# Kernel optimization log

Measured on AMD Instinct MI355X. Metric: run time of the kernel, lower is better.

The kernel has to match this reference:

```python
import jax, jax.numpy as jnp
import numpy as np

B, N, D = 16, 2048, 256  # batch (pairs*2), num_keypoints, descriptor_dim


def setup_inputs() -> dict:
    key = jax.random.key(0)
    k1, k2, k3, k4 = jax.random.split(key, 4)
    descriptors = jax.random.normal(k1, (B, N, D), dtype=jnp.float32)
    mask = jax.random.randint(k2, (B, N), 0, 2, dtype=jnp.int32)
    proj_w = jax.random.normal(k3, (D, D), dtype=jnp.float32) * 0.02
    proj_b = jnp.zeros((D,), dtype=jnp.float32)
    match_w = jax.random.normal(k4, (1, D), dtype=jnp.float32) * 0.02
    match_b = jnp.zeros((1,), dtype=jnp.float32)
    return {"descriptors": descriptors, "mask": mask, "proj_w": proj_w,
            "proj_b": proj_b, "match_w": match_w, "match_b": match_b}


def reference(descriptors, mask, proj_w, proj_b, match_w, match_b):
    batch, n, d = descriptors.shape
    pairs = batch // 2
    # final projection + temperature scaling
    m_desc = (descriptors @ proj_w.T + proj_b) / jnp.asarray(d, descriptors.dtype) ** 0.25
    m_desc = m_desc.reshape(pairs, 2, n, d)
    # similarity: [pairs, n0, n1]
    similarity = jnp.einsum('bnd,bmd->bnm', m_desc[:, 0], m_desc[:, 1])
    mask_p = mask.reshape(pairs, 2, n)
    pair_mask = mask_p[:, 0][:, :, None] * mask_p[:, 1][:, None, :]
    neg_min = jnp.finfo(similarity.dtype).min
    similarity = jnp.where(pair_mask == 0, neg_min, similarity)
    # matchability logits: [B, n, 1] -> split per pair
    matchability = (descriptors @ match_w.T + match_b).reshape(pairs, 2, n)
    m0 = matchability[:, 0]  # [pairs, n]
    m1 = matchability[:, 1]  # [pairs, n]
    certainties = jax.nn.log_sigmoid(m0)[:, :, None] + jax.nn.log_sigmoid(m1)[:, None, :]
    scores0 = jax.nn.log_softmax(similarity, axis=2)
    scores1 = jax.nn.log_softmax(similarity, axis=1)
    inner = scores0 + scores1 + certainties
    scores = jnp.zeros((pairs, n + 1, n + 1), dtype=similarity.dtype)
    scores = scores.at[:, :n, :n].set(inner)
    scores = scores.at[:, :-1, -1].set(jax.nn.log_sigmoid(-m0))
    scores = scores.at[:, -1, :-1].set(jax.nn.log_sigmoid(-m1))
    return scores
```

## Files before the change

kernel.cpp:

```cpp
#include <hip/hip_runtime.h>
#include <math.h>

typedef unsigned short u16;
typedef __attribute__((ext_vector_type(8))) short bf16x8;
typedef __attribute__((ext_vector_type(4))) float f32x4;

#define N 2048
#define D 256
#define PAIRS 8
#define NO 2049
#define NEGMIN  -3.40282347e38f
#define MASKVAL -3.0e38f
#define LDA 72
#define LDST 136

#define WS_LS0   0
#define WS_LS1   (1*PAIRS*N)
#define WS_LSN0  (2*PAIRS*N)
#define WS_LSN1  (3*PAIRS*N)
#define WS_RMAX  (4*PAIRS*N)
#define WS_RLSE  (5*PAIRS*N)
#define WS_CMAX  (6*PAIRS*N)
#define WS_CLSE  (7*PAIRS*N)
#define WS_RPM   (8*PAIRS*N)
#define WS_RPS   (WS_RPM + PAIRS*16*N)
#define WS_CPM   (WS_RPS + PAIRS*16*N)
#define WS_CPS   (WS_CPM + PAIRS*16*N)
#define WS_F_COUNT (WS_CPS + PAIRS*16*N)

__device__ __forceinline__ float b2f(u16 u) {
    return __uint_as_float(((unsigned)u) << 16);
}
__device__ __forceinline__ u16 f2b(float f) {
    unsigned x = __float_as_uint(f);
    x += 0x7FFFu + ((x >> 16) & 1u);
    return (u16)(x >> 16);
}
__device__ __forceinline__ unsigned pk2(float a, float b) {
    return (unsigned)f2b(a) | ((unsigned)f2b(b) << 16);
}
__device__ __forceinline__ float logsig(float x) {
    return fminf(x, 0.f) - log1pf(expf(-fabsf(x)));
}
__device__ __forceinline__ void online1(float& m, float& s, float x) {
    float nm = fmaxf(m, x);
    float e = __expf(fminf(m, x) - nm);
    s = (x > m) ? s * e + 1.f : s + e;
    m = nm;
}
__device__ __forceinline__ void onmerge(float& m, float& s, float om, float os) {
    float nm = fmaxf(m, om);
    s = s * __expf(m - nm) + os * __expf(om - nm);
    m = nm;
}
__device__ __forceinline__ void gl_lds16(const u16* g, u16* l) {
    __builtin_amdgcn_global_load_lds(
        (const __attribute__((address_space(1))) unsigned*)(const void*)g,
        (__attribute__((address_space(3))) unsigned*)(void*)l, 16, 0, 0);
}

__global__ __launch_bounds__(256) void k_proj_mfma(const float* __restrict__ A,
                                                   const float* __restrict__ W,
                                                   const float* __restrict__ bias,
                                                   const float* __restrict__ mw,
                                                   const float* __restrict__ mb,
                                                   u16* __restrict__ mdesc,
                                                   float* __restrict__ wsf) {
    __shared__ union {
        struct { u16 A[128 * LDA]; u16 B[128 * LDA]; } t;
        u16 stage[128][LDST];
    } sh;
    int r0 = blockIdx.x * 128, c0 = blockIdx.y * 128;
    int tid = threadIdx.x;
    int w = tid >> 6, lane = tid & 63;
    int ln = lane & 15, q = lane >> 4;
    int wr0 = (w >> 1) * 64, wc0 = (w & 1) * 64;
    f32x4 zero = {0.f, 0.f, 0.f, 0.f};
    f32x4 acc[4][4];
    #pragma unroll
    for (int a = 0; a < 4; ++a)
        #pragma unroll
        for (int b = 0; b < 4; ++b) acc[a][b] = zero;
    float mdot[4] = {0.f, 0.f, 0.f, 0.f};
    int domatch = (blockIdx.y == 0);

    for (int kb = 0; kb < D; kb += 64) {
        __syncthreads();
        #pragma unroll
        for (int t = 0; t < 4; ++t) {
            int c = t * 256 + tid;
            int row = c >> 3, part = c & 7;
            const float* ap = A + (size_t)(r0 + row) * D + kb + part * 8;
            float4 f0 = *(const float4*)ap;
            float4 f1 = *(const float4*)(ap + 4);
            uint4 va;
            va.x = pk2(f0.x, f0.y); va.y = pk2(f0.z, f0.w);
            va.z = pk2(f1.x, f1.y); va.w = pk2(f1.z, f1.w);
            *(uint4*)&sh.t.A[row * LDA + part * 8] = va;
            if (domatch) {
                float4 w0 = *(const float4*)(mw + kb + part * 8);
                float4 w1 = *(const float4*)(mw + kb + part * 8 + 4);
                mdot[t] += f0.x*w0.x + f0.y*w0.y + f0.z*w0.z + f0.w*w0.w
                         + f1.x*w1.x + f1.y*w1.y + f1.z*w1.z + f1.w*w1.w;
            }
            const float* bp = W + (size_t)(c0 + row) * D + kb + part * 8;
            float4 g0 = *(const float4*)bp;
            float4 g1 = *(const float4*)(bp + 4);
            uint4 vb;
            vb.x = pk2(g0.x, g0.y); vb.y = pk2(g0.z, g0.w);
            vb.z = pk2(g1.x, g1.y); vb.w = pk2(g1.z, g1.w);
            *(uint4*)&sh.t.B[row * LDA + part * 8] = vb;
        }
        __syncthreads();
        #pragma unroll
        for (int kk = 0; kk < 64; kk += 32) {
            bf16x8 af[4], bf[4];
            #pragma unroll
            for (int ri = 0; ri < 4; ++ri)
                af[ri] = *(const bf16x8*)&sh.t.A[(wr0 + ri*16 + ln) * LDA + kk + q*8];
            #pragma unroll
            for (int ci = 0; ci < 4; ++ci)
                bf[ci] = *(const bf16x8*)&sh.t.B[(wc0 + ci*16 + ln) * LDA + kk + q*8];
            #pragma unroll
            for (int ri = 0; ri < 4; ++ri)
                #pragma unroll
                for (int ci = 0; ci < 4; ++ci)
                    acc[ri][ci] = __builtin_amdgcn_mfma_f32_16x16x32_bf16(af[ri], bf[ci], acc[ri][ci], 0, 0, 0);
        }
    }
    if (domatch) {
        #pragma unroll
        for (int t = 0; t < 4; ++t) {
            float s = mdot[t];
            s += __shfl_xor(s, 1, 64);
            s += __shfl_xor(s, 2, 64);
            s += __shfl_xor(s, 4, 64);
            if ((tid & 7) == 0) {
                int row_g = r0 + t * 32 + (tid >> 3);
                float m = s + mb[0];
                int b = row_g >> 11;
                int i = row_g & (N - 1);
                int pp = b >> 1, sid = b & 1;
                float ls = logsig(m), lsn = logsig(-m);
                if (sid == 0) { wsf[WS_LS0 + pp*N + i] = ls; wsf[WS_LSN0 + pp*N + i] = lsn; }
                else          { wsf[WS_LS1 + pp*N + i] = ls; wsf[WS_LSN1 + pp*N + i] = lsn; }
            }
        }
    }
    __syncthreads();
    #pragma unroll
    for (int ri = 0; ri < 4; ++ri) {
        #pragma unroll
        for (int reg = 0; reg < 4; ++reg) {
            int row_l = wr0 + ri*16 + q*4 + reg;
            #pragma unroll
            for (int ci = 0; ci < 4; ++ci) {
                int col = c0 + wc0 + ci*16 + ln;
                float v = (acc[ri][ci][reg] + bias[col]) * 0.25f;
                sh.stage[row_l][wc0 + ci*16 + ln] = f2b(v);
            }
        }
    }
    __syncthreads();
    {
        int row_l = tid >> 1, half = tid & 1;
        u16* dp = mdesc + (size_t)(r0 + row_l) * D + c0 + half * 64;
        const u16* lp = &sh.stage[row_l][half * 64];
        #pragma unroll
        for (int i = 0; i < 8; ++i)
            *(uint4*)(dp + i * 8) = *(const uint4*)(lp + i * 8);
    }
}

__global__ __launch_bounds__(256) void k_sim_mfma(const u16* __restrict__ mdesc,
                                                  const int* __restrict__ mask,
                                                  u16* __restrict__ sim,
                                                  float* __restrict__ wsf) {
    __shared__ union {
        u16 lds[4][128 * 64];
        u16 stage[128][LDST];
    } sh;
    __shared__ float rpm[128][2], rps[128][2];
    __shared__ float cpm[128][2], cps[128][2];
    int p = blockIdx.z;
    const u16* Am = mdesc + (size_t)(2*p) * N * D;
    const u16* Bm = mdesc + (size_t)(2*p + 1) * N * D;
    int r0 = blockIdx.x * 128, c0 = blockIdx.y * 128;
    int tid = threadIdx.x;
    int w = tid >> 6, lane = tid & 63;
    int ln = lane & 15, q = lane >> 4;
    int wr0 = (w >> 1) * 64, wc0 = (w & 1) * 64;
    int rsub = lane >> 3;
    int scol = (((lane & 7) ^ rsub) << 3);
    f32x4 zero = {0.f, 0.f, 0.f, 0.f};
    f32x4 acc[4][4];
    #pragma unroll
    for (int a = 0; a < 4; ++a)
        #pragma unroll
        for (int b = 0; b < 4; ++b) acc[a][b] = zero;

    #define STAGE(t_, bufi_) do {                                               \
        int kb_ = (t_) * 64;                                                    \
        u16* Ad_ = &sh.lds[(bufi_)*2][0];                                       \
        u16* Bd_ = &sh.lds[(bufi_)*2+1][0];                                     \
        _Pragma("unroll")                                                       \
        for (int j_ = 0; j_ < 4; ++j_) {                                        \
            int row_ = w * 32 + j_ * 8 + rsub;                                  \
            gl_lds16(Am + (size_t)(r0 + row_) * D + kb_ + scol,                 \
                     Ad_ + (w * 32 + j_ * 8) * 64);                             \
            gl_lds16(Bm + (size_t)(c0 + row_) * D + kb_ + scol,                 \
                     Bd_ + (w * 32 + j_ * 8) * 64);                             \
        }                                                                       \
    } while (0)

    STAGE(0, 0);
    __syncthreads();
    #pragma unroll
    for (int t = 0; t < 4; ++t) {
        int cur = t & 1;
        if (t < 3) STAGE(t + 1, cur ^ 1);
        const char* Abase = (const char*)&sh.lds[cur*2][0];
        const char* Bbase = (const char*)&sh.lds[cur*2+1][0];
        #pragma unroll
        for (int kk = 0; kk < 64; kk += 32) {
            bf16x8 af[4], bf[4];
            int cbase = kk * 2 + q * 16;
            int cswz = cbase ^ ((ln & 7) << 4);
            #pragma unroll
            for (int ri = 0; ri < 4; ++ri) {
                int row = wr0 + ri*16 + ln;
                af[ri] = *(const bf16x8*)(Abase + row * 128 + cswz);
            }
            #pragma unroll
            for (int ci = 0; ci < 4; ++ci) {
                int row = wc0 + ci*16 + ln;
                bf[ci] = *(const bf16x8*)(Bbase + row * 128 + cswz);
            }
            #pragma unroll
            for (int ri = 0; ri < 4; ++ri)
                #pragma unroll
                for (int ci = 0; ci < 4; ++ci)
                    acc[ri][ci] = __builtin_amdgcn_mfma_f32_16x16x32_bf16(af[ri], bf[ci], acc[ri][ci], 0, 0, 0);
        }
        __syncthreads();
    }
    #undef STAGE

    const int* m0 = mask + (size_t)(2*p) * N;
    const int* m1 = mask + (size_t)(2*p + 1) * N;
    int mcol[4];
    #pragma unroll
    for (int ci = 0; ci < 4; ++ci) mcol[ci] = m1[c0 + wc0 + ci*16 + ln];
    #pragma unroll
    for (int ri = 0; ri < 4; ++ri) {
        #pragma unroll
        for (int reg = 0; reg < 4; ++reg) {
            int row_l = wr0 + ri*16 + q*4 + reg;
            int mr = m0[r0 + row_l];
            #pragma unroll
            for (int ci = 0; ci < 4; ++ci) {
                float v = (mr && mcol[ci]) ? acc[ri][ci][reg] : MASKVAL;
                acc[ri][ci][reg] = v;
                sh.stage[row_l][wc0 + ci*16 + ln] = f2b(v);
            }
        }
    }
    #pragma unroll
    for (int ri = 0; ri < 4; ++ri) {
        #pragma unroll
        for (int reg = 0; reg < 4; ++reg) {
            float x0 = acc[ri][0][reg], x1 = acc[ri][1][reg];
            float x2 = acc[ri][2][reg], x3 = acc[ri][3][reg];
            float m = fmaxf(fmaxf(x0, x1), fmaxf(x2, x3));
            #pragma unroll
            for (int off = 1; off <= 8; off <<= 1)
                m = fmaxf(m, __shfl_xor(m, off, 64));
            float s = __expf(x0 - m) + __expf(x1 - m) + __expf(x2 - m) + __expf(x3 - m);
            #pragma unroll
            for (int off = 1; off <= 8; off <<= 1)
                s += __shfl_xor(s, off, 64);
            if (ln == 0) {
                int rl = wr0 + ri*16 + q*4 + reg;
                rpm[rl][w & 1] = m; rps[rl][w & 1] = s;
            }
        }
    }
    #pragma unroll
    for (int ci = 0; ci < 4; ++ci) {
        float m = acc[0][ci][0];
        #pragma unroll
        for (int ri = 0; ri < 4; ++ri)
            #pragma unroll
            for (int reg = 0; reg < 4; ++reg)
                if (!(ri == 0 && reg == 0)) m = fmaxf(m, acc[ri][ci][reg]);
        #pragma unroll
        for (int off = 16; off <= 32; off <<= 1)
            m = fmaxf(m, __shfl_xor(m, off, 64));
        float s = 0.f;
        #pragma unroll
        for (int ri = 0; ri < 4; ++ri)
            #pragma unroll
            for (int reg = 0; reg < 4; ++reg)
                s += __expf(acc[ri][ci][reg] - m);
        #pragma unroll
        for (int off = 16; off <= 32; off <<= 1)
            s += __shfl_xor(s, off, 64);
        if (q == 0) {
            int cl = wc0 + ci*16 + ln;
            cpm[cl][w >> 1] = m; cps[cl][w >> 1] = s;
        }
    }
    __syncthreads();
    {
        int row_l = tid >> 1, half = tid & 1;
        u16* sp = sim + ((size_t)p * N + r0 + row_l) * N + c0 + half * 64;
        const u16* lp = &sh.stage[row_l][half * 64];
        #pragma unroll
        for (int i = 0; i < 8; ++i)
            *(uint4*)(sp + i * 8) = *(const uint4*)(lp + i * 8);
    }
    if (tid < 128) {
        float m = rpm[tid][0], s = rps[tid][0];
        onmerge(m, s, rpm[tid][1], rps[tid][1]);
        size_t o = (size_t)(p * 16 + blockIdx.y) * N + r0 + tid;
        wsf[WS_RPM + o] = m; wsf[WS_RPS + o] = s;
    } else {
        int c = tid - 128;
        float m = cpm[c][0], s = cps[c][0];
        onmerge(m, s, cpm[c][1], cps[c][1]);
        size_t o = (size_t)(p * 16 + blockIdx.x) * N + c0 + c;
        wsf[WS_CPM + o] = m;
        wsf[WS_CPS + o] = s;
    }
}

__global__ __launch_bounds__(256) void k_red(float* __restrict__ wsf) {
    int i = blockIdx.x * 256 + threadIdx.x;
    int p = blockIdx.y;
    float m = wsf[WS_CPM + (size_t)(p*16) * N + i];
    float s = wsf[WS_CPS + (size_t)(p*16) * N + i];
    #pragma unroll
    for (int rb = 1; rb < 16; ++rb)
        onmerge(m, s, wsf[WS_CPM + (size_t)(p*16 + rb) * N + i],
                      wsf[WS_CPS + (size_t)(p*16 + rb) * N + i]);
    wsf[WS_CMAX + p * N + i] = m;
    wsf[WS_CLSE + p * N + i] = logf(s);
}

__global__ __launch_bounds__(256) void k_final(u16* __restrict__ out,
                                               const u16* __restrict__ sim,
                                               const float* __restrict__ wsf) {
    int strip = blockIdx.x;
    int p = blockIdx.y;
    int tid = threadIdx.x;
    __shared__ float rm_l[8], rl_l[8], l0_l[8], ln0_l[8];
    if (tid < 128) {
        int r = tid >> 4, cb = tid & 15;
        int i = strip * 8 + r;
        if (i < N) {
            float m = wsf[WS_RPM + (size_t)(p*16 + cb) * N + i];
            float sv = wsf[WS_RPS + (size_t)(p*16 + cb) * N + i];
            #pragma unroll
            for (int off = 1; off <= 8; off <<= 1) {
                float om = __shfl_xor(m, off, 64);
                float os = __shfl_xor(sv, off, 64);
                onmerge(m, sv, om, os);
            }
            if (cb == 0) {
                rm_l[r]  = m;
                rl_l[r]  = logf(sv);
                l0_l[r]  = wsf[WS_LS0  + p*N + i];
                ln0_l[r] = wsf[WS_LSN0 + p*N + i];
            }
        }
    }
    __syncthreads();
    unsigned* up = (unsigned*)out;
    #pragma unroll
    for (int k = 0; k < 4; ++k) {
        int kk = k * 256 + tid;
        int jc = 2 * kk;
        float cm0 = wsf[WS_CMAX + p*N + jc];
        float cl0 = wsf[WS_CLSE + p*N + jc];
        float s10 = wsf[WS_LS1  + p*N + jc];
        float cm1 = wsf[WS_CMAX + p*N + jc + 1];
        float cl1 = wsf[WS_CLSE + p*N + jc + 1];
        float s11 = wsf[WS_LS1  + p*N + jc + 1];
        float cm2 = 0.f, cl2 = 0.f, s12 = 0.f;
        if (jc + 2 < N) {
            cm2 = wsf[WS_CMAX + p*N + jc + 2];
            cl2 = wsf[WS_CLSE + p*N + jc + 2];
            s12 = wsf[WS_LS1  + p*N + jc + 2];
        }
        for (int r = 0; r < 8; ++r) {
            int i = strip * 8 + r;
            if (i > N) break;
            size_t B0 = ((size_t)p * NO + i) * NO;
            int head = (p + i) & 1;
            size_t U0 = (B0 + head) >> 1;
            if (i == N) {
                int j0 = 2*kk + head;
                float o0 = (j0 < N) ? wsf[WS_LSN1 + p*N + j0] : 0.f;
                int j1 = j0 + 1;
                float o1 = (j1 < N) ? wsf[WS_LSN1 + p*N + j1] : 0.f;
                up[U0 + kk] = pk2(o0, o1);
                if (tid == 0 && k == 0) {
                    if (head) out[B0] = f2b(wsf[WS_LSN1 + p*N]);
                    else      out[B0 + N] = 0;
                }
                continue;
            }
            float rm = rm_l[r], rl = rl_l[r], l0 = l0_l[r], ln0 = ln0_l[r];
            const u16* srow = sim + ((size_t)p * N + i) * N;
            unsigned a = *(const unsigned*)(srow + jc);
            float o0, o1;
            if (head) {
                float x0 = b2f((u16)(a >> 16));
                float a0 = (x0 - rm) - rl;
                float b0 = (x0 - cm1) - cl1;
                o0 = fmaxf(fmaxf(a0 + b0, MASKVAL) + (l0 + s11), MASKVAL);
                if (jc + 2 < N) {
                    float x1 = b2f(srow[jc + 2]);
                    float a1 = (x1 - rm) - rl;
                    float b1 = (x1 - cm2) - cl2;
                    o1 = fmaxf(fmaxf(a1 + b1, MASKVAL) + (l0 + s12), MASKVAL);
                } else {
                    o1 = ln0;
                }
            } else {
                float x0 = b2f((u16)a);
                float a0 = (x0 - rm) - rl;
                float b0 = (x0 - cm0) - cl0;
                o0 = fmaxf(fmaxf(a0 + b0, MASKVAL) + (l0 + s10), MASKVAL);
                float x1 = b2f((u16)(a >> 16));
                float a1 = (x1 - rm) - rl;
                float b1 = (x1 - cm1) - cl1;
                o1 = fmaxf(fmaxf(a1 + b1, MASKVAL) + (l0 + s11), MASKVAL);
            }
            up[U0 + kk] = pk2(o0, o1);
            if (tid == 0 && k == 0) {
                if (head) {
                    float x = b2f(srow[0]);
                    float aa = (x - rm) - rl;
                    float bb = (x - wsf[WS_CMAX + p*N]) - wsf[WS_CLSE + p*N];
                    out[B0] = f2b(fmaxf(fmaxf(aa + bb, MASKVAL) + (l0 + wsf[WS_LS1 + p*N]), MASKVAL));
                } else {
                    out[B0 + N] = f2b(ln0);
                }
            }
        }
    }
}

extern "C" void kernel_launch(void* const* d_in, const int* in_sizes, int n_in,
                              void* d_out, int out_size, void* d_ws, size_t ws_size,
                              hipStream_t stream) {
    const float* desc    = (const float*)d_in[0];
    const int*   mask    = (const int*)d_in[1];
    const float* proj_w  = (const float*)d_in[2];
    const float* proj_b  = (const float*)d_in[3];
    const float* match_w = (const float*)d_in[4];
    const float* match_b = (const float*)d_in[5];
    u16*   out = (u16*)d_out;
    float* wsf = (float*)d_ws;
    u16*   mdesc = (u16*)((char*)d_ws + (size_t)WS_F_COUNT * sizeof(float));
    u16*   simw  = mdesc + (size_t)16 * N * D;

    k_proj_mfma<<<dim3(256, 2),    256, 0, stream>>>(desc, proj_w, proj_b, match_w, match_b, mdesc, wsf);
    k_sim_mfma <<<dim3(16, 16, 8), 256, 0, stream>>>(mdesc, mask, simw, wsf);
    k_red      <<<dim3(8, 8),      256, 0, stream>>>(wsf);
    k_final    <<<dim3(257, 8),    256, 0, stream>>>(out, simw, wsf);
}
```

Baseline: 275.9 us.

## Precompute packed row/column stats and stage final output through LDS

The row-partial merge moves from k_final into k_red, which now also writes packed per-row (neg max-lse, ls0, lsn0) and per-column (neg max-lse, ls1) records so k_final loads vectorised structs instead of many scattered scalars. k_final reads the bf16 similarity with 16-byte loads, computes 8 outputs per thread, stages them in LDS to handle the odd row alignment of the 2049-wide output, then writes aligned 32-bit stores. The last output row is handled by a dedicated strip branch. This adds LDS use and a barrier per block and makes k_red do more work.

```diff
diff --git a/kernel.cpp b/kernel.cpp
--- a/kernel.cpp
+++ b/kernel.cpp
@@ -18,15 +18,13 @@
 #define WS_LS1   (1*PAIRS*N)
 #define WS_LSN0  (2*PAIRS*N)
 #define WS_LSN1  (3*PAIRS*N)
-#define WS_RMAX  (4*PAIRS*N)
-#define WS_RLSE  (5*PAIRS*N)
-#define WS_CMAX  (6*PAIRS*N)
-#define WS_CLSE  (7*PAIRS*N)
+#define WS_CST   (6*PAIRS*N)
 #define WS_RPM   (8*PAIRS*N)
 #define WS_RPS   (WS_RPM + PAIRS*16*N)
 #define WS_CPM   (WS_RPS + PAIRS*16*N)
 #define WS_CPS   (WS_CPM + PAIRS*16*N)
-#define WS_F_COUNT (WS_CPS + PAIRS*16*N)
+#define WS_ROW   (WS_CPS + PAIRS*16*N)
+#define WS_F_COUNT (WS_ROW + 4*PAIRS*N)
 
 __device__ __forceinline__ float b2f(u16 u) {
     return __uint_as_float(((unsigned)u) << 16);
@@ -41,12 +39,6 @@
 }
 __device__ __forceinline__ float logsig(float x) {
     return fminf(x, 0.f) - log1pf(expf(-fabsf(x)));
-}
-__device__ __forceinline__ void online1(float& m, float& s, float x) {
-    float nm = fmaxf(m, x);
-    float e = __expf(fminf(m, x) - nm);
-    s = (x > m) ? s * e + 1.f : s + e;
-    m = nm;
 }
 __device__ __forceinline__ void onmerge(float& m, float& s, float om, float os) {
     float nm = fmaxf(m, om);
@@ -343,8 +335,22 @@
     for (int rb = 1; rb < 16; ++rb)
         onmerge(m, s, wsf[WS_CPM + (size_t)(p*16 + rb) * N + i],
                       wsf[WS_CPS + (size_t)(p*16 + rb) * N + i]);
-    wsf[WS_CMAX + p * N + i] = m;
-    wsf[WS_CLSE + p * N + i] = logf(s);
+    float2 cpack;
+    cpack.x = -m - logf(s);
+    cpack.y = wsf[WS_LS1 + p*N + i];
+    *(float2*)&wsf[WS_CST + ((size_t)p * N + i) * 2] = cpack;
+    float rm = wsf[WS_RPM + (size_t)(p*16) * N + i];
+    float rs = wsf[WS_RPS + (size_t)(p*16) * N + i];
+    #pragma unroll
+    for (int rb = 1; rb < 16; ++rb)
+        onmerge(rm, rs, wsf[WS_RPM + (size_t)(p*16 + rb) * N + i],
+                        wsf[WS_RPS + (size_t)(p*16 + rb) * N + i]);
+    float4 rpack;
+    rpack.x = -rm - logf(rs);
+    rpack.y = wsf[WS_LS0  + p*N + i];
+    rpack.z = wsf[WS_LSN0 + p*N + i];
+    rpack.w = 0.f;
+    *(float4*)&wsf[WS_ROW + ((size_t)p * N + i) * 4] = rpack;
 }
 
 __global__ __launch_bounds__(256) void k_final(u16* __restrict__ out,
@@ -353,101 +359,79 @@
     int strip = blockIdx.x;
     int p = blockIdx.y;
     int tid = threadIdx.x;
-    __shared__ float rm_l[8], rl_l[8], l0_l[8], ln0_l[8];
-    if (tid < 128) {
-        int r = tid >> 4, cb = tid & 15;
+    unsigned* up = (unsigned*)out;
+    if (strip == 256) {
+        int head = p & 1;
+        size_t B0 = ((size_t)p * NO + N) * NO;
+        size_t U0 = (B0 + head) >> 1;
+        const float* lsn1 = wsf + WS_LSN1 + p * N;
+        #pragma unroll
+        for (int k = 0; k < 4; ++k) {
+            int kk = k * 256 + tid;
+            int j0 = head + 2 * kk;
+            float o0 = (j0 < N) ? lsn1[j0] : 0.f;
+            float o1 = (j0 + 1 < N) ? lsn1[j0 + 1] : 0.f;
+            up[U0 + kk] = pk2(o0, o1);
+        }
+        if (tid == 0) {
+            if (head) out[B0] = f2b(lsn1[0]);
+            else      out[B0 + N] = 0;
+        }
+        return;
+    }
+    __shared__ u16 stg[8][2052];
+    int c8 = tid * 8;
+    const float* cst = wsf + WS_CST + ((size_t)p * N + c8) * 2;
+    float4 cs[4];
+    #pragma unroll
+    for (int k = 0; k < 4; ++k) cs[k] = *(const float4*)(cst + 4 * k);
+    #pragma unroll
+    for (int r = 0; r < 8; ++r) {
         int i = strip * 8 + r;
-        if (i < N) {
-            float m = wsf[WS_RPM + (size_t)(p*16 + cb) * N + i];
-            float sv = wsf[WS_RPS + (size_t)(p*16 + cb) * N + i];
-            #pragma unroll
-            for (int off = 1; off <= 8; off <<= 1) {
-                float om = __shfl_xor(m, off, 64);
-                float os = __shfl_xor(sv, off, 64);
-                onmerge(m, sv, om, os);
-            }
-            if (cb == 0) {
-                rm_l[r]  = m;
-                rl_l[r]  = logf(sv);
-                l0_l[r]  = wsf[WS_LS0  + p*N + i];
-                ln0_l[r] = wsf[WS_LSN0 + p*N + i];
-            }
-        }
+        int head = (p + i) & 1;
+        float4 rsv = *(const float4*)&wsf[WS_ROW + ((size_t)p * N + i) * 4];
+        float rc = rsv.x, l0 = rsv.y, ln0 = rsv.z;
+        uint4 v = *(const uint4*)(sim + ((size_t)p * N + i) * N + c8);
+        unsigned vv[4] = {v.x, v.y, v.z, v.w};
+        float o[8];
+        #pragma unroll
+        for (int k = 0; k < 8; ++k) {
+            float x = b2f((u16)(vv[k >> 1] >> ((k & 1) * 16)));
+            float cA = ((const float*)&cs[0])[2 * k];
+            float s1 = ((const float*)&cs[0])[2 * k + 1];
+            float t = (x + rc) + (x + cA);
+            o[k] = fmaxf(fmaxf(t, MASKVAL) + (l0 + s1), MASKVAL);
+        }
+        if (!head) {
+            uint4 wv;
+            wv.x = pk2(o[0], o[1]); wv.y = pk2(o[2], o[3]);
+            wv.z = pk2(o[4], o[5]); wv.w = pk2(o[6], o[7]);
+            *(uint4*)&stg[r][c8] = wv;
+        } else {
+            stg[r][c8 + 1] = f2b(o[0]);
+            *(unsigned*)&stg[r][c8 + 2] = pk2(o[1], o[2]);
+            *(unsigned*)&stg[r][c8 + 4] = pk2(o[3], o[4]);
+            *(unsigned*)&stg[r][c8 + 6] = pk2(o[5], o[6]);
+            stg[r][c8 + 8] = f2b(o[7]);
+        }
+        if (tid == 255) stg[r][2048 + head] = f2b(ln0);
     }
     __syncthreads();
-    unsigned* up = (unsigned*)out;
-    #pragma unroll
-    for (int k = 0; k < 4; ++k) {
-        int kk = k * 256 + tid;
-        int jc = 2 * kk;
-        float cm0 = wsf[WS_CMAX + p*N + jc];
-        float cl0 = wsf[WS_CLSE + p*N + jc];
-        float s10 = wsf[WS_LS1  + p*N + jc];
-        float cm1 = wsf[WS_CMAX + p*N + jc + 1];
-        float cl1 = wsf[WS_CLSE + p*N + jc + 1];
-        float s11 = wsf[WS_LS1  + p*N + jc + 1];
-        float cm2 = 0.f, cl2 = 0.f, s12 = 0.f;
-        if (jc + 2 < N) {
-            cm2 = wsf[WS_CMAX + p*N + jc + 2];
-            cl2 = wsf[WS_CLSE + p*N + jc + 2];
-            s12 = wsf[WS_LS1  + p*N + jc + 2];
-        }
-        for (int r = 0; r < 8; ++r) {
-            int i = strip * 8 + r;
-            if (i > N) break;
-            size_t B0 = ((size_t)p * NO + i) * NO;
-            int head = (p + i) & 1;
-            size_t U0 = (B0 + head) >> 1;
-            if (i == N) {
-                int j0 = 2*kk + head;
-                float o0 = (j0 < N) ? wsf[WS_LSN1 + p*N + j0] : 0.f;
-                int j1 = j0 + 1;
-                float o1 = (j1 < N) ? wsf[WS_LSN1 + p*N + j1] : 0.f;
-                up[U0 + kk] = pk2(o0, o1);
-                if (tid == 0 && k == 0) {
-                    if (head) out[B0] = f2b(wsf[WS_LSN1 + p*N]);
-                    else      out[B0 + N] = 0;
-                }
-                continue;
-            }
-            float rm = rm_l[r], rl = rl_l[r], l0 = l0_l[r], ln0 = ln0_l[r];
-            const u16* srow = sim + ((size_t)p * N + i) * N;
-            unsigned a = *(const unsigned*)(srow + jc);
-            float o0, o1;
-            if (head) {
-                float x0 = b2f((u16)(a >> 16));
-                float a0 = (x0 - rm) - rl;
-                float b0 = (x0 - cm1) - cl1;
-                o0 = fmaxf(fmaxf(a0 + b0, MASKVAL) + (l0 + s11), MASKVAL);
-                if (jc + 2 < N) {
-                    float x1 = b2f(srow[jc + 2]);
-                    float a1 = (x1 - rm) - rl;
-                    float b1 = (x1 - cm2) - cl2;
-                    o1 = fmaxf(fmaxf(a1 + b1, MASKVAL) + (l0 + s12), MASKVAL);
-                } else {
-                    o1 = ln0;
-                }
-            } else {
-                float x0 = b2f((u16)a);
-                float a0 = (x0 - rm) - rl;
-                float b0 = (x0 - cm0) - cl0;
-                o0 = fmaxf(fmaxf(a0 + b0, MASKVAL) + (l0 + s10), MASKVAL);
-                float x1 = b2f((u16)(a >> 16));
-                float a1 = (x1 - rm) - rl;
-                float b1 = (x1 - cm1) - cl1;
-                o1 = fmaxf(fmaxf(a1 + b1, MASKVAL) + (l0 + s11), MASKVAL);
-            }
-            up[U0 + kk] = pk2(o0, o1);
-            if (tid == 0 && k == 0) {
-                if (head) {
-                    float x = b2f(srow[0]);
-                    float aa = (x - rm) - rl;
-                    float bb = (x - wsf[WS_CMAX + p*N]) - wsf[WS_CLSE + p*N];
-                    out[B0] = f2b(fmaxf(fmaxf(aa + bb, MASKVAL) + (l0 + wsf[WS_LS1 + p*N]), MASKVAL));
-                } else {
-                    out[B0 + N] = f2b(ln0);
-                }
-            }
+    #pragma unroll
+    for (int r = 0; r < 8; ++r) {
+        int i = strip * 8 + r;
+        int head = (p + i) & 1;
+        size_t B0 = ((size_t)p * NO + i) * NO;
+        size_t U0 = (B0 + head) >> 1;
+        const unsigned* srow32 = (const unsigned*)&stg[r][0];
+        #pragma unroll
+        for (int k = 0; k < 4; ++k) {
+            int kk = k * 256 + tid;
+            up[U0 + kk] = srow32[kk + head];
+        }
+        if (tid == 0) {
+            if (head) out[B0] = stg[r][1];
+            else      out[B0 + N] = stg[r][2048];
         }
     }
 }
```

Measured after the change: 257.6 us. 1.07x faster.
